# Kernel tuning notes

Hardware: AMD Instinct MI355X
Metric: run time of the kernel (lower is better)

The kernel has to match this reference:

```python
import jax, jax.numpy as jnp
import numpy as np

B, S, R = 8, 4096, 512
E, K, ATOMS, XAR, TOPK = 64, 256, 16, 3, 2
TEMP = 1.0


def setup_inputs() -> dict:
    key = jax.random.key(0)
    k0, k1, k2, k3, k4 = jax.random.split(key, 5)
    x_latent = jax.random.normal(k0, (B, S, R), jnp.float32)
    router_w = jax.random.normal(k1, (E, R), jnp.float32) * (1.0 / np.sqrt(R))
    atoms = jax.random.normal(k2, (E, ATOMS, R), jnp.float32) * 0.01
    combo_weights = jax.random.uniform(k3, (E, K, XAR), jnp.float32) * 0.5 + 0.25
    combo_logits = jax.random.normal(k4, (E, K, XAR, ATOMS), jnp.float32) * 0.01
    return {"x_latent": x_latent, "router_w": router_w, "atoms": atoms,
            "combo_weights": combo_weights, "combo_logits": combo_logits}


def _expert_centroids(atoms, combo_weights, combo_logits):
    # Hard codeword path (vectorized over experts):
    # sign atoms -> pick argmax atom per (k, xor slot) -> weight -> sum -> sign -> mean over k
    binary = jnp.sign(atoms)                                   # [E, A, R]
    # softmax(logits/t) then argmax == argmax(logits) (monotone)
    idx = jnp.argmax(combo_logits, axis=-1)                    # [E, K, XAR]
    sel = binary[jnp.arange(E)[:, None, None], idx]            # [E, K, XAR, R]
    codewords = jnp.sign((sel * combo_weights[..., None]).sum(axis=2))  # [E, K, R]
    return codewords.mean(axis=1)                              # [E, R]


def reference(x_latent, router_w, atoms, combo_weights, combo_logits):
    t = max(TEMP, 0.1)
    router_logits = jnp.einsum('bsr,er->bse', x_latent, router_w)   # [B, S, E]
    probs_t = jax.nn.softmax(router_logits / t, axis=-1)
    gates, expert_ids = jax.lax.top_k(probs_t, TOPK)                # [B, S, 2]
    gates = gates / gates.sum(axis=-1, keepdims=True)

    centroids = _expert_centroids(atoms, combo_weights, combo_logits)  # [E, R]

    # aux load-balancing loss (uses untempered softmax)
    router_prob = jax.nn.softmax(router_logits, axis=-1)
    aux_loss = E * jnp.sum(router_prob.mean(axis=(0, 1)) *
                           (router_prob > 0).astype(x_latent.dtype).mean(axis=(0, 1)))

    # dense per-expert gate = sum over topk slots of gate * (id == e), then combine with centroids
    dense_gates = (jax.nn.one_hot(expert_ids, E, dtype=gates.dtype) *
                   gates[..., None]).sum(axis=-2)                    # [B, S, E]
    combined = jnp.einsum('bse,er->bsr', dense_gates, centroids)     # [B, S, R]
    return combined, aux_loss
```

## Files before the change

### kernel.cpp

```cpp
#include <hip/hip_runtime.h>
#include <math.h>

#define TOKENS 32768
#define RDIM 512
#define NEXP 64
#define NK 256
#define LDQ 136
#define PSTR 67
#define TAU 4.0e-3f

typedef unsigned short u16;
typedef float f32x4 __attribute__((ext_vector_type(4)));
typedef short s16x8 __attribute__((ext_vector_type(8)));

#define MFMA_B16(a, b, c) __builtin_amdgcn_mfma_f32_16x16x32_bf16(a, b, c, 0, 0, 0)

__device__ __forceinline__ void split_pack(float4 v, unsigned& h01, unsigned& h23,
                                           unsigned& l01, unsigned& l23) {
    unsigned u0 = __float_as_uint(v.x), u1 = __float_as_uint(v.y);
    unsigned u2 = __float_as_uint(v.z), u3 = __float_as_uint(v.w);
    float r0 = v.x - __uint_as_float(u0 & 0xFFFF0000u);
    float r1 = v.y - __uint_as_float(u1 & 0xFFFF0000u);
    float r2 = v.z - __uint_as_float(u2 & 0xFFFF0000u);
    float r3 = v.w - __uint_as_float(u3 & 0xFFFF0000u);
    h01 = (u0 >> 16) | (u1 & 0xFFFF0000u);
    h23 = (u2 >> 16) | (u3 & 0xFFFF0000u);
    l01 = (__float_as_uint(r0) >> 16) | (__float_as_uint(r1) & 0xFFFF0000u);
    l23 = (__float_as_uint(r2) >> 16) | (__float_as_uint(r3) & 0xFFFF0000u);
}

__device__ __forceinline__ void split8(float4 a, float4 b, s16x8& hi, s16x8& lo) {
    union U { unsigned u[4]; s16x8 v; };
    U H, L;
    split_pack(a, H.u[0], H.u[1], L.u[0], L.u[1]);
    split_pack(b, H.u[2], H.u[3], L.u[2], L.u[3]);
    hi = H.v; lo = L.v;
}

__device__ __forceinline__ void centroid_body(
    int e, int half, int tid,
    const float* __restrict__ atoms, const float* __restrict__ cw,
    const float* __restrict__ cl, float* __restrict__ cent, unsigned* pack)
{
    {
        const int k = tid;
        unsigned u = 0;
        float w3[3];
        #pragma unroll
        for (int xx = 0; xx < 3; ++xx) {
            const float* cp = cl + ((((size_t)e * NK + k) * 3 + xx) << 4);
            float v[16];
            *(float4*)(v + 0)  = *(const float4*)(cp + 0);
            *(float4*)(v + 4)  = *(const float4*)(cp + 4);
            *(float4*)(v + 8)  = *(const float4*)(cp + 8);
            *(float4*)(v + 12) = *(const float4*)(cp + 12);
            float best = v[0]; int bi = 0;
            #pragma unroll
            for (int a = 1; a < 16; ++a) {
                if (v[a] > best) { best = v[a]; bi = a; }
            }
            u |= (unsigned)bi << (4 * xx);
            w3[xx] = cw[((size_t)e * NK + k) * 3 + xx];
        }
        unsigned lut = 0;
        #pragma unroll
        for (int c = 0; c < 8; ++c) {
            float val = ((c & 1) ? -w3[0] : w3[0])
                      + ((c & 2) ? -w3[1] : w3[1])
                      + ((c & 4) ? -w3[2] : w3[2]);
            lut |= (val < 0.f ? 1u : 0u) << c;
        }
        pack[k] = u | (lut << 16);
    }

    const int r = half * 256 + tid;
    unsigned B0 = 0;
    #pragma unroll
    for (int a = 0; a < 16; ++a)
        B0 |= (atoms[((size_t)e * 16 + a) * RDIM + r] < 0.f ? 1u : 0u) << a;
    __syncthreads();

    int n0 = 0;
    #pragma unroll 2
    for (int k = 0; k < NK; k += 8) {
        unsigned pk8[8];
        #pragma unroll
        for (int j = 0; j < 8; ++j) pk8[j] = pack[k + j];
        #pragma unroll
        for (int j = 0; j < 8; ++j) {
            unsigned u  = pk8[j];
            unsigned i0 = u & 15u, i1 = (u >> 4) & 15u, i2 = (u >> 8) & 15u;
            unsigned c0 = ((B0 >> i0) & 1u) | (((B0 >> i1) & 1u) << 1) | (((B0 >> i2) & 1u) << 2);
            n0 += (u >> (16 + c0)) & 1u;
        }
    }
    cent[(size_t)e * RDIM + r] = 1.f - (float)n0 * (1.f / 128.f);
}

__global__ __launch_bounds__(256) void centroid_pack_kernel(
    const float* __restrict__ atoms,
    const float* __restrict__ cw,
    const float* __restrict__ cl,
    const float* __restrict__ w,
    float* __restrict__ cent,
    u16* __restrict__ pk_hi,
    u16* __restrict__ pk_lo,
    float* __restrict__ aux_sum,
    unsigned* __restrict__ aux_cnt)
{
    __shared__ unsigned pack[NK];
    const int tid = threadIdx.x;
    if (blockIdx.x == 0 && tid < 64) { aux_sum[tid] = 0.f; aux_cnt[tid] = 0u; }

    if (blockIdx.x < 128) {
        centroid_body(blockIdx.x >> 1, blockIdx.x & 1, tid, atoms, cw, cl, cent, pack);
    } else {
        const int gid = (blockIdx.x - 128) * 256 + tid;
        const int row = gid >> 7;
        const int k0  = (gid & 127) * 4;
        const int g   = k0 >> 5, kg = (k0 >> 3) & 3, j = k0 & 7;
        const int idx = ((g * 4 + kg) * 64 + row) * 8 + j;
        float4 wv = *(const float4*)(w + (size_t)row * RDIM + k0);
        unsigned h01, h23, l01, l23;
        split_pack(wv, h01, h23, l01, l23);
        *(uint2*)&pk_hi[idx] = make_uint2(h01, h23);
        *(uint2*)&pk_lo[idx] = make_uint2(l01, l23);
    }
}

__global__ __launch_bounds__(128, 4) void moe_fast(
    const float* __restrict__ x,
    const u16* __restrict__ pk_hi,
    const u16* __restrict__ pk_lo,
    const float* __restrict__ w,
    const float* __restrict__ cent,
    float* __restrict__ out,
    float* __restrict__ aux_sum,
    unsigned* __restrict__ aux_cnt)
{
    __shared__ float P[32 * PSTR];
    __shared__ float candv[32 * 13];
    __shared__ int   candi[32 * 13];
    __shared__ float qsum[32 * 5];
    __shared__ float gateL[32 * 4];
    __shared__ float s_aux[64];
    __shared__ unsigned s_cnt[64];

    const int tid  = threadIdx.x;
    const int lane = tid & 63;
    const int wv   = tid >> 6;
    const int l15  = lane & 15;
    const int kq   = lane >> 4;
    const int kgrp = kq << 3;
    const int tok0 = blockIdx.x * 32;

    if (tid < 64) { s_aux[tid] = 0.f; s_cnt[tid] = 0u; }

    f32x4 acc[4];
    #pragma unroll
    for (int nt = 0; nt < 4; ++nt) acc[nt] = (f32x4){0.f, 0.f, 0.f, 0.f};

    const float* xlane = x + (size_t)(tok0 + wv * 16 + l15) * RDIM + kgrp;
    const int fbase = kq * 512 + l15 * 8;

    float4 pA[2], pB[2];
    pA[0] = *(const float4*)(xlane);      pB[0] = *(const float4*)(xlane + 4);
    pA[1] = *(const float4*)(xlane + 32); pB[1] = *(const float4*)(xlane + 36);

    #pragma unroll
    for (int g = 0; g < 16; ++g) {
        s16x8 ah, al;
        split8(pA[g & 1], pB[g & 1], ah, al);
        if (g + 2 < 16) {
            const float* nx = xlane + (g + 2) * 32;
            pA[g & 1] = *(const float4*)(nx);
            pB[g & 1] = *(const float4*)(nx + 4);
        }
        const u16* ph = pk_hi + g * 2048 + fbase;
        const u16* pl = pk_lo + g * 2048 + fbase;
        #pragma unroll
        for (int nt = 0; nt < 4; ++nt) {
            s16x8 bh = *(const s16x8*)(ph + nt * 128);
            s16x8 bl = *(const s16x8*)(pl + nt * 128);
            acc[nt] = MFMA_B16(ah, bh, acc[nt]);
            acc[nt] = MFMA_B16(ah, bl, acc[nt]);
            acc[nt] = MFMA_B16(al, bh, acc[nt]);
        }
    }

    #pragma unroll
    for (int nt = 0; nt < 4; ++nt)
        #pragma unroll
        for (int i = 0; i < 4; ++i)
            P[(wv * 16 + (kq << 2) + i) * PSTR + nt * 16 + l15] = acc[nt][i];
    __syncthreads();

    const int tt = tid & 31;
    const int ss = tid >> 5;
    float v[16];
    #pragma unroll
    for (int j = 0; j < 16; ++j) v[j] = P[tt * PSTR + ss * 16 + j];

    float m1 = -INFINITY, m2 = -INFINITY, m3 = -INFINITY;
    int   i1 = NEXP, i2 = NEXP, i3 = NEXP;
    #pragma unroll
    for (int j = 0; j < 16; ++j) {
        float val = v[j]; int e = ss * 16 + j;
        if (val > m1)      { m3 = m2; i3 = i2; m2 = m1; i2 = i1; m1 = val; i1 = e; }
        else if (val > m2) { m3 = m2; i3 = i2; m2 = val; i2 = e; }
        else if (val > m3) { m3 = val; i3 = e; }
    }
    candv[tt * 13 + ss * 3 + 0] = m1; candi[tt * 13 + ss * 3 + 0] = i1;
    candv[tt * 13 + ss * 3 + 1] = m2; candi[tt * 13 + ss * 3 + 1] = i2;
    candv[tt * 13 + ss * 3 + 2] = m3; candi[tt * 13 + ss * 3 + 2] = i3;
    __syncthreads();

    m1 = m2 = m3 = -INFINITY; i1 = i2 = i3 = NEXP;
    #pragma unroll
    for (int q = 0; q < 12; ++q) {
        float val = candv[tt * 13 + q]; int e = candi[tt * 13 + q];
        if (val > m1)      { m3 = m2; i3 = i2; m2 = m1; i2 = i1; m1 = val; i1 = e; }
        else if (val > m2) { m3 = m2; i3 = i2; m2 = val; i2 = e; }
        else if (val > m3) { m3 = val; i3 = e; }
    }

    float ex[16]; float ps = 0.f;
    #pragma unroll
    for (int j = 0; j < 16; ++j) { ex[j] = __expf(v[j] - m1); ps += ex[j]; }
    qsum[tt * 5 + ss] = ps;

    if (wv == 0) {
        if (lane < 32) {
            const float ed  = __expf(m2 - m1);
            const float inv = 1.f / (1.f + ed);
            gateL[tt * 4 + 0] = inv;
            gateL[tt * 4 + 1] = ed * inv;
            ((int*)gateL)[tt * 4 + 2] = i1;
            ((int*)gateL)[tt * 4 + 3] = i2;
        }
        unsigned long long bmask = __ballot(lane < 32 && (m2 - m3 < TAU));
        while (bmask) {
            const int f = __ffsll(bmask) - 1;
            bmask &= bmask - 1;
            int id3[3];
            id3[0] = __shfl(i1, f); id3[1] = __shfl(i2, f); id3[2] = __shfl(i3, f);
            const float* xrow = x + (size_t)(tok0 + f) * RDIM + lane * 8;
            float4 a0 = *(const float4*)(xrow);
            float4 a1 = *(const float4*)(xrow + 4);
            float d[3];
            #pragma unroll
            for (int jj = 0; jj < 3; ++jj) {
                const float* wrow = w + (size_t)id3[jj] * RDIM + lane * 8;
                float4 b0 = *(const float4*)(wrow);
                float4 b1 = *(const float4*)(wrow + 4);
                float p = a0.x * b0.x;
                p = fmaf(a0.y, b0.y, p); p = fmaf(a0.z, b0.z, p); p = fmaf(a0.w, b0.w, p);
                p = fmaf(a1.x, b1.x, p); p = fmaf(a1.y, b1.y, p);
                p = fmaf(a1.z, b1.z, p); p = fmaf(a1.w, b1.w, p);
                #pragma unroll
                for (int off = 32; off; off >>= 1) p += __shfl_xor(p, off);
                d[jj] = p;
            }
            int b = 0;
            if (d[1] > d[0] || (d[1] == d[0] && id3[1] < id3[0])) b = 1;
            if (d[2] > d[b] || (d[2] == d[b] && id3[2] < id3[b])) b = 2;
            int sec;
            if (b == 0)      sec = (d[1] > d[2] || (d[1] == d[2] && id3[1] < id3[2])) ? 1 : 2;
            else if (b == 1) sec = (d[0] > d[2] || (d[0] == d[2] && id3[0] < id3[2])) ? 0 : 2;
            else             sec = (d[0] > d[1] || (d[0] == d[1] && id3[0] < id3[1])) ? 0 : 1;
            if (lane == f) {
                const float ed  = __expf(d[sec] - d[b]);
                const float inv = 1.f / (1.f + ed);
                gateL[f * 4 + 0] = inv;
                gateL[f * 4 + 1] = ed * inv;
                ((int*)gateL)[f * 4 + 2] = id3[b];
                ((int*)gateL)[f * 4 + 3] = id3[sec];
            }
        }
    }
    __syncthreads();

    float Z = 0.f;
    #pragma unroll
    for (int k = 0; k < 4; ++k) Z += qsum[tt * 5 + k];
    const float invZ = 1.f / Z;
    #pragma unroll
    for (int j = 0; j < 16; ++j) P[tt * PSTR + ss * 16 + j] = ex[j] * invZ;
    __syncthreads();

    {
        const int e = tid & 63, tq = tid >> 6;
        float s = 0.f; unsigned cn = 0u;
        #pragma unroll
        for (int t = 0; t < 16; ++t) {
            float pv = P[(tq * 16 + t) * PSTR + e];
            s += pv; cn += (pv > 0.f) ? 1u : 0u;
        }
        atomicAdd(&s_aux[e], s);
        atomicAdd(&s_cnt[e], cn);
    }
    __syncthreads();
    if (tid < 64) {
        atomicAdd(aux_sum + tid, s_aux[tid]);
        atomicAdd(aux_cnt + tid, s_cnt[tid]);
    }

    {
        const int e = lane;
        #pragma unroll
        for (int s2 = 0; s2 < 16; ++s2) {
            const int t2 = wv * 16 + s2;
            float4 g4 = *(float4*)&gateL[t2 * 4];
            const float g1 = g4.x, g2 = g4.y;
            const int e1 = __float_as_int(g4.z), e2 = __float_as_int(g4.w);
            const float4* c1 = (const float4*)(cent + (size_t)e1 * RDIM);
            const float4* c2 = (const float4*)(cent + (size_t)e2 * RDIM);
            float4* op = (float4*)(out + (size_t)(tok0 + t2) * RDIM);
            float4 A0 = c1[e],      Bb0 = c2[e];
            float4 A1 = c1[e + 64], Bb1 = c2[e + 64];
            float4 o0, o1;
            o0.x = fmaf(g1, A0.x, g2 * Bb0.x); o0.y = fmaf(g1, A0.y, g2 * Bb0.y);
            o0.z = fmaf(g1, A0.z, g2 * Bb0.z); o0.w = fmaf(g1, A0.w, g2 * Bb0.w);
            o1.x = fmaf(g1, A1.x, g2 * Bb1.x); o1.y = fmaf(g1, A1.y, g2 * Bb1.y);
            o1.z = fmaf(g1, A1.z, g2 * Bb1.z); o1.w = fmaf(g1, A1.w, g2 * Bb1.w);
            op[e]      = o0;
            op[e + 64] = o1;
        }
    }
}

__global__ __launch_bounds__(256) void centroid_kernel(
    const float* __restrict__ atoms,
    const float* __restrict__ cw,
    const float* __restrict__ cl,
    float* __restrict__ cent,
    float* __restrict__ aux_sum,
    unsigned* __restrict__ aux_cnt)
{
    __shared__ unsigned pack[NK];
    const int tid = threadIdx.x;
    if (blockIdx.x == 0 && tid < 64) { aux_sum[tid] = 0.f; aux_cnt[tid] = 0u; }
    centroid_body(blockIdx.x >> 1, blockIdx.x & 1, tid, atoms, cw, cl, cent, pack);
}

__global__ __launch_bounds__(256, 4) void moe_main(
    const float* __restrict__ x,
    const float* __restrict__ w,
    const float* __restrict__ cent,
    float* __restrict__ out,
    float* __restrict__ aux_sum,
    unsigned* __restrict__ aux_cnt)
{
    __shared__ u16 wlds[2 * 64 * LDQ];
    u16* whi = wlds;
    u16* wlo = wlds + 64 * LDQ;
    float* P     = (float*)wlds;
    float* candv = P + 64 * PSTR;
    int*   candi = (int*)(candv + 64 * 13);
    float* qsum  = (float*)(candi + 64 * 13);
    float* gateL = qsum + 64 * 5;
    __shared__ float s_aux[64];
    __shared__ unsigned s_cnt[64];

    const int tid  = threadIdx.x;
    const int lane = tid & 63;
    const int wave = tid >> 6;
    const int l15  = lane & 15;
    const int kgrp = (lane >> 4) << 3;
    const int tok0 = blockIdx.x * 64;

    if (tid < 64) { s_aux[tid] = 0.f; s_cnt[tid] = 0u; }

    f32x4 acc[4];
    #pragma unroll
    for (int nt = 0; nt < 4; ++nt) acc[nt] = (f32x4){0.f, 0.f, 0.f, 0.f};

    const float* xlane = x + (size_t)(tok0 + wave * 16 + l15) * RDIM + kgrp;
    const int wrow = tid >> 2;
    const int wseg = tid & 3;
    const float* wg = w + (size_t)wrow * RDIM + wseg * 32;
    const int woff = wrow * LDQ + wseg * 32;

    float4 preA[4], preB[4];
    #pragma unroll
    for (int i = 0; i < 4; ++i) {
        preA[i] = *(const float4*)(xlane + i * 32);
        preB[i] = *(const float4*)(xlane + i * 32 + 4);
    }

    #pragma unroll
    for (int q = 0; q < 4; ++q) {
        if (q) __syncthreads();
        {
            const float* wq = wg + q * 128;
            uint2 h2[2], l2[2];
            #pragma unroll
            for (int j = 0; j < 8; ++j) {
                float4 wvv = *(const float4*)(wq + j * 4);
                split_pack(wvv, h2[j & 1].x, h2[j & 1].y, l2[j & 1].x, l2[j & 1].y);
                if (j & 1) {
                    *(uint4*)&whi[woff + (j - 1) * 4] =
                        make_uint4(h2[0].x, h2[0].y, h2[1].x, h2[1].y);
                    *(uint4*)&wlo[woff + (j - 1) * 4] =
                        make_uint4(l2[0].x, l2[0].y, l2[1].x, l2[1].y);
                }
            }
        }
        __syncthreads();

        #pragma unroll
        for (int kb = 0; kb < 4; ++kb) {
            const int g = q * 4 + kb;
            s16x8 ah, al;
            split8(preA[g & 3], preB[g & 3], ah, al);
            if (g + 4 < 16) {
                const float* nx = xlane + (g + 4) * 32;
                preA[g & 3] = *(const float4*)(nx);
                preB[g & 3] = *(const float4*)(nx + 4);
            }
            const int kl = kb * 32 + kgrp;
            #pragma unroll
            for (int nt = 0; nt < 4; ++nt) {
                const int brow = nt * 16 + l15;
                s16x8 bh = *(const s16x8*)&whi[brow * LDQ + kl];
                s16x8 bl = *(const s16x8*)&wlo[brow * LDQ + kl];
                acc[nt] = MFMA_B16(ah, bh, acc[nt]);
                acc[nt] = MFMA_B16(ah, bl, acc[nt]);
                acc[nt] = MFMA_B16(al, bh, acc[nt]);
            }
        }
    }

    __syncthreads();
    #pragma unroll
    for (int nt = 0; nt < 4; ++nt)
        #pragma unroll
        for (int i = 0; i < 4; ++i)
            P[(wave * 16 + ((lane >> 4) << 2) + i) * PSTR + nt * 16 + l15] = acc[nt][i];
    __syncthreads();

    const int tt = tid & 63;
    const int ss = tid >> 6;
    float v[16];
    #pragma unroll
    for (int j = 0; j < 16; ++j) v[j] = P[tt * PSTR + ss * 16 + j];

    float m1 = -INFINITY, m2 = -INFINITY, m3 = -INFINITY;
    int   i1 = NEXP, i2 = NEXP, i3 = NEXP;
    #pragma unroll
    for (int j = 0; j < 16; ++j) {
        float val = v[j]; int e = ss * 16 + j;
        if (val > m1)      { m3 = m2; i3 = i2; m2 = m1; i2 = i1; m1 = val; i1 = e; }
        else if (val > m2) { m3 = m2; i3 = i2; m2 = val; i2 = e; }
        else if (val > m3) { m3 = val; i3 = e; }
    }
    candv[tt * 13 + ss * 3 + 0] = m1; candi[tt * 13 + ss * 3 + 0] = i1;
    candv[tt * 13 + ss * 3 + 1] = m2; candi[tt * 13 + ss * 3 + 1] = i2;
    candv[tt * 13 + ss * 3 + 2] = m3; candi[tt * 13 + ss * 3 + 2] = i3;
    __syncthreads();

    m1 = m2 = m3 = -INFINITY; i1 = i2 = i3 = NEXP;
    #pragma unroll
    for (int q = 0; q < 12; ++q) {
        float val = candv[tt * 13 + q]; int e = candi[tt * 13 + q];
        if (val > m1)      { m3 = m2; i3 = i2; m2 = m1; i2 = i1; m1 = val; i1 = e; }
        else if (val > m2) { m3 = m2; i3 = i2; m2 = val; i2 = e; }
        else if (val > m3) { m3 = val; i3 = e; }
    }

    float ex[16]; float ps = 0.f;
    #pragma unroll
    for (int j = 0; j < 16; ++j) { ex[j] = __expf(v[j] - m1); ps += ex[j]; }
    qsum[tt * 5 + ss] = ps;

    if (ss == 0) {
        {
            const float ed  = __expf(m2 - m1);
            const float inv = 1.f / (1.f + ed);
            gateL[tt * 4 + 0] = inv;
            gateL[tt * 4 + 1] = ed * inv;
            ((int*)gateL)[tt * 4 + 2] = i1;
            ((int*)gateL)[tt * 4 + 3] = i2;
        }
        unsigned long long bmask = __ballot(m2 - m3 < TAU);
        while (bmask) {
            const int f = __ffsll(bmask) - 1;
            bmask &= bmask - 1;
            int id3[3];
            id3[0] = __shfl(i1, f); id3[1] = __shfl(i2, f); id3[2] = __shfl(i3, f);
            const float* xrow = x + (size_t)(tok0 + f) * RDIM + lane * 8;
            float4 a0 = *(const float4*)(xrow);
            float4 a1 = *(const float4*)(xrow + 4);
            float d[3];
            #pragma unroll
            for (int jj = 0; jj < 3; ++jj) {
                const float* wrow2 = w + (size_t)id3[jj] * RDIM + lane * 8;
                float4 b0 = *(const float4*)(wrow2);
                float4 b1 = *(const float4*)(wrow2 + 4);
                float p = a0.x * b0.x;
                p = fmaf(a0.y, b0.y, p); p = fmaf(a0.z, b0.z, p); p = fmaf(a0.w, b0.w, p);
                p = fmaf(a1.x, b1.x, p); p = fmaf(a1.y, b1.y, p);
                p = fmaf(a1.z, b1.z, p); p = fmaf(a1.w, b1.w, p);
                #pragma unroll
                for (int off = 32; off; off >>= 1) p += __shfl_xor(p, off);
                d[jj] = p;
            }
            int b = 0;
            if (d[1] > d[0] || (d[1] == d[0] && id3[1] < id3[0])) b = 1;
            if (d[2] > d[b] || (d[2] == d[b] && id3[2] < id3[b])) b = 2;
            int sec;
            if (b == 0)      sec = (d[1] > d[2] || (d[1] == d[2] && id3[1] < id3[2])) ? 1 : 2;
            else if (b == 1) sec = (d[0] > d[2] || (d[0] == d[2] && id3[0] < id3[2])) ? 0 : 2;
            else             sec = (d[0] > d[1] || (d[0] == d[1] && id3[0] < id3[1])) ? 0 : 1;
            if (lane == f) {
                const float ed  = __expf(d[sec] - d[b]);
                const float inv = 1.f / (1.f + ed);
                gateL[f * 4 + 0] = inv;
                gateL[f * 4 + 1] = ed * inv;
                ((int*)gateL)[f * 4 + 2] = id3[b];
                ((int*)gateL)[f * 4 + 3] = id3[sec];
            }
        }
    }
    __syncthreads();

    float Z = 0.f;
    #pragma unroll
    for (int k = 0; k < 4; ++k) Z += qsum[tt * 5 + k];
    const float invZ = 1.f / Z;
    #pragma unroll
    for (int j = 0; j < 16; ++j) P[tt * PSTR + ss * 16 + j] = ex[j] * invZ;
    __syncthreads();

    {
        const int e = tid & 63, tq = tid >> 6;
        float s = 0.f; unsigned cn = 0u;
        #pragma unroll
        for (int t = 0; t < 16; ++t) {
            float pv = P[(tq * 16 + t) * PSTR + e];
            s += pv; cn += (pv > 0.f) ? 1u : 0u;
        }
        atomicAdd(&s_aux[e], s);
        atomicAdd(&s_cnt[e], cn);
    }
    __syncthreads();
    if (tid < 64) {
        atomicAdd(aux_sum + tid, s_aux[tid]);
        atomicAdd(aux_cnt + tid, s_cnt[tid]);
    }

    {
        const int e = lane;
        #pragma unroll
        for (int s2 = 0; s2 < 16; ++s2) {
            const int t2 = wave * 16 + s2;
            float4 g4 = *(float4*)&gateL[t2 * 4];
            const float g1 = g4.x, g2 = g4.y;
            const int e1 = __float_as_int(g4.z), e2 = __float_as_int(g4.w);
            const float4* c1 = (const float4*)(cent + (size_t)e1 * RDIM);
            const float4* c2 = (const float4*)(cent + (size_t)e2 * RDIM);
            float4* op = (float4*)(out + (size_t)(tok0 + t2) * RDIM);
            float4 A0 = c1[e],      Bb0 = c2[e];
            float4 A1 = c1[e + 64], Bb1 = c2[e + 64];
            float4 o0, o1;
            o0.x = fmaf(g1, A0.x, g2 * Bb0.x); o0.y = fmaf(g1, A0.y, g2 * Bb0.y);
            o0.z = fmaf(g1, A0.z, g2 * Bb0.z); o0.w = fmaf(g1, A0.w, g2 * Bb0.w);
            o1.x = fmaf(g1, A1.x, g2 * Bb1.x); o1.y = fmaf(g1, A1.y, g2 * Bb1.y);
            o1.z = fmaf(g1, A1.z, g2 * Bb1.z); o1.w = fmaf(g1, A1.w, g2 * Bb1.w);
            op[e]      = o0;
            op[e + 64] = o1;
        }
    }
}

__global__ __launch_bounds__(64) void aux_kernel(
    const float* __restrict__ sums,
    const unsigned* __restrict__ cnts,
    float* __restrict__ out_aux)
{
    const int e = threadIdx.x;
    float v = (sums[e] * (1.f / (float)TOKENS)) * ((float)cnts[e] * (1.f / (float)TOKENS));
    #pragma unroll
    for (int off = 32; off; off >>= 1) v += __shfl_xor(v, off);
    if (e == 0) out_aux[0] = (float)NEXP * v;
}

extern "C" void kernel_launch(void* const* d_in, const int* in_sizes, int n_in,
                              void* d_out, int out_size, void* d_ws, size_t ws_size,
                              hipStream_t stream) {
    const float* x     = (const float*)d_in[0];
    const float* rw    = (const float*)d_in[1];
    const float* atoms = (const float*)d_in[2];
    const float* cwts  = (const float*)d_in[3];
    const float* clog  = (const float*)d_in[4];
    float* out = (float*)d_out;
    float* out_aux = out + (size_t)TOKENS * RDIM;

    float*    aux_sum = (float*)d_ws;
    unsigned* aux_cnt = (unsigned*)((char*)d_ws + 256);
    float*    cent    = (float*)((char*)d_ws + 512);
    u16*      pk_hi   = (u16*)((char*)d_ws + 512 + 131072);
    u16*      pk_lo   = (u16*)((char*)d_ws + 512 + 131072 + 65536);
    const bool fast = ws_size >= (size_t)(512 + 131072 + 2 * 65536);

    if (fast) {
        centroid_pack_kernel<<<160, 256, 0, stream>>>(atoms, cwts, clog, rw, cent,
                                                      pk_hi, pk_lo, aux_sum, aux_cnt);
        moe_fast<<<1024, 128, 0, stream>>>(x, pk_hi, pk_lo, rw, cent, out, aux_sum, aux_cnt);
    } else {
        centroid_kernel<<<128, 256, 0, stream>>>(atoms, cwts, clog, cent, aux_sum, aux_cnt);
        moe_main<<<512, 256, 0, stream>>>(x, rw, cent, out, aux_sum, aux_cnt);
    }
    aux_kernel<<<1, 64, 0, stream>>>(aux_sum, aux_cnt, out_aux);
}
```

Before: 168.1 us.

## Split router GEMM expert columns across waves with 16-token blocks

Blocks now cover 16 tokens instead of 32, and each of four waves computes a 16-expert slice of the router logits rather than all 64 experts for its own tokens. The grid grows to 2048 blocks of 256 threads to raise occupancy and shorten each wave's serial MFMA chain. Top-k, softmax and the near-tie refinement now run in a single wave per block, and exponentials are recomputed instead of kept in registers. The cost is that all four waves load the same x rows, relying on cache to absorb the duplicate reads, and the other three waves sit idle during the top-k phase.

```diff
diff --git a/kernel.cpp b/kernel.cpp
--- a/kernel.cpp
+++ b/kernel.cpp
@@ -128,7 +128,7 @@
     }
 }
 
-__global__ __launch_bounds__(128, 4) void moe_fast(
+__global__ __launch_bounds__(256, 8) void moe_fast2(
     const float* __restrict__ x,
     const u16* __restrict__ pk_hi,
     const u16* __restrict__ pk_lo,
@@ -138,11 +138,11 @@
     float* __restrict__ aux_sum,
     unsigned* __restrict__ aux_cnt)
 {
-    __shared__ float P[32 * PSTR];
-    __shared__ float candv[32 * 13];
-    __shared__ int   candi[32 * 13];
-    __shared__ float qsum[32 * 5];
-    __shared__ float gateL[32 * 4];
+    __shared__ float P[16 * PSTR];
+    __shared__ float candv[16 * 13];
+    __shared__ int   candi[16 * 13];
+    __shared__ float qsum[16 * 4];
+    __shared__ float gateL[16 * 4];
     __shared__ float s_aux[64];
     __shared__ unsigned s_cnt[64];
 
@@ -152,16 +152,14 @@
     const int l15  = lane & 15;
     const int kq   = lane >> 4;
     const int kgrp = kq << 3;
-    const int tok0 = blockIdx.x * 32;
+    const int tok0 = blockIdx.x * 16;
 
     if (tid < 64) { s_aux[tid] = 0.f; s_cnt[tid] = 0u; }
 
-    f32x4 acc[4];
-    #pragma unroll
-    for (int nt = 0; nt < 4; ++nt) acc[nt] = (f32x4){0.f, 0.f, 0.f, 0.f};
-
-    const float* xlane = x + (size_t)(tok0 + wv * 16 + l15) * RDIM + kgrp;
-    const int fbase = kq * 512 + l15 * 8;
+    f32x4 acc = (f32x4){0.f, 0.f, 0.f, 0.f};
+
+    const float* xlane = x + (size_t)(tok0 + l15) * RDIM + kgrp;
+    const int fbase = kq * 512 + (wv * 16 + l15) * 8;
 
     float4 pA[2], pB[2];
     pA[0] = *(const float4*)(xlane);      pB[0] = *(const float4*)(xlane + 4);
@@ -178,59 +176,53 @@
         }
         const u16* ph = pk_hi + g * 2048 + fbase;
         const u16* pl = pk_lo + g * 2048 + fbase;
-        #pragma unroll
-        for (int nt = 0; nt < 4; ++nt) {
-            s16x8 bh = *(const s16x8*)(ph + nt * 128);
-            s16x8 bl = *(const s16x8*)(pl + nt * 128);
-            acc[nt] = MFMA_B16(ah, bh, acc[nt]);
-            acc[nt] = MFMA_B16(ah, bl, acc[nt]);
-            acc[nt] = MFMA_B16(al, bh, acc[nt]);
-        }
-    }
-
-    #pragma unroll
-    for (int nt = 0; nt < 4; ++nt)
-        #pragma unroll
-        for (int i = 0; i < 4; ++i)
-            P[(wv * 16 + (kq << 2) + i) * PSTR + nt * 16 + l15] = acc[nt][i];
-    __syncthreads();
-
-    const int tt = tid & 31;
-    const int ss = tid >> 5;
-    float v[16];
-    #pragma unroll
-    for (int j = 0; j < 16; ++j) v[j] = P[tt * PSTR + ss * 16 + j];
-
-    float m1 = -INFINITY, m2 = -INFINITY, m3 = -INFINITY;
-    int   i1 = NEXP, i2 = NEXP, i3 = NEXP;
-    #pragma unroll
-    for (int j = 0; j < 16; ++j) {
-        float val = v[j]; int e = ss * 16 + j;
-        if (val > m1)      { m3 = m2; i3 = i2; m2 = m1; i2 = i1; m1 = val; i1 = e; }
-        else if (val > m2) { m3 = m2; i3 = i2; m2 = val; i2 = e; }
-        else if (val > m3) { m3 = val; i3 = e; }
-    }
-    candv[tt * 13 + ss * 3 + 0] = m1; candi[tt * 13 + ss * 3 + 0] = i1;
-    candv[tt * 13 + ss * 3 + 1] = m2; candi[tt * 13 + ss * 3 + 1] = i2;
-    candv[tt * 13 + ss * 3 + 2] = m3; candi[tt * 13 + ss * 3 + 2] = i3;
-    __syncthreads();
-
-    m1 = m2 = m3 = -INFINITY; i1 = i2 = i3 = NEXP;
-    #pragma unroll
-    for (int q = 0; q < 12; ++q) {
-        float val = candv[tt * 13 + q]; int e = candi[tt * 13 + q];
-        if (val > m1)      { m3 = m2; i3 = i2; m2 = m1; i2 = i1; m1 = val; i1 = e; }
-        else if (val > m2) { m3 = m2; i3 = i2; m2 = val; i2 = e; }
-        else if (val > m3) { m3 = val; i3 = e; }
-    }
-
-    float ex[16]; float ps = 0.f;
-    #pragma unroll
-    for (int j = 0; j < 16; ++j) { ex[j] = __expf(v[j] - m1); ps += ex[j]; }
-    qsum[tt * 5 + ss] = ps;
-
-    if (wv == 0) {
-        if (lane < 32) {
+        s16x8 bh = *(const s16x8*)ph;
+        s16x8 bl = *(const s16x8*)pl;
+        acc = MFMA_B16(ah, bh, acc);
+        acc = MFMA_B16(ah, bl, acc);
+        acc = MFMA_B16(al, bh, acc);
+    }
+
+    #pragma unroll
+    for (int i = 0; i < 4; ++i)
+        P[(kq * 4 + i) * PSTR + wv * 16 + l15] = acc[i];
+    __syncthreads();
+
+    if (tid < 64) {
+        const int tt = lane & 15;
+        const int ss = lane >> 4;
+        float v[16];
+        #pragma unroll
+        for (int j = 0; j < 16; ++j) v[j] = P[tt * PSTR + ss * 16 + j];
+
+        float m1 = -INFINITY, m2 = -INFINITY, m3 = -INFINITY;
+        int   i1 = NEXP, i2 = NEXP, i3 = NEXP;
+        #pragma unroll
+        for (int j = 0; j < 16; ++j) {
+            float val = v[j]; int e = ss * 16 + j;
+            if (val > m1)      { m3 = m2; i3 = i2; m2 = m1; i2 = i1; m1 = val; i1 = e; }
+            else if (val > m2) { m3 = m2; i3 = i2; m2 = val; i2 = e; }
+            else if (val > m3) { m3 = val; i3 = e; }
+        }
+        candv[tt * 13 + ss * 3 + 0] = m1; candi[tt * 13 + ss * 3 + 0] = i1;
+        candv[tt * 13 + ss * 3 + 1] = m2; candi[tt * 13 + ss * 3 + 1] = i2;
+        candv[tt * 13 + ss * 3 + 2] = m3; candi[tt * 13 + ss * 3 + 2] = i3;
+
+        m1 = m2 = m3 = -INFINITY; i1 = i2 = i3 = NEXP;
+        #pragma unroll
+        for (int q = 0; q < 12; ++q) {
+            float val = candv[tt * 13 + q]; int e = candi[tt * 13 + q];
+            if (val > m1)      { m3 = m2; i3 = i2; m2 = m1; i2 = i1; m1 = val; i1 = e; }
+            else if (val > m2) { m3 = m2; i3 = i2; m2 = val; i2 = e; }
+            else if (val > m3) { m3 = val; i3 = e; }
+        }
+
+        float ps = 0.f;
+        #pragma unroll
+        for (int j = 0; j < 16; ++j) ps += __expf(v[j] - m1);
+        qsum[tt * 4 + ss] = ps;
+
+        if (ss == 0) {
             const float ed  = __expf(m2 - m1);
             const float inv = 1.f / (1.f + ed);
             gateL[tt * 4 + 0] = inv;
@@ -238,7 +230,7 @@
             ((int*)gateL)[tt * 4 + 2] = i1;
             ((int*)gateL)[tt * 4 + 3] = i2;
         }
-        unsigned long long bmask = __ballot(lane < 32 && (m2 - m3 < TAU));
+        unsigned long long bmask = __ballot(ss == 0 && (m2 - m3 < TAU));
         while (bmask) {
             const int f = __ffsll(bmask) - 1;
             bmask &= bmask - 1;
@@ -277,23 +269,21 @@
                 ((int*)gateL)[f * 4 + 3] = id3[sec];
             }
         }
-    }
-    __syncthreads();
-
-    float Z = 0.f;
-    #pragma unroll
-    for (int k = 0; k < 4; ++k) Z += qsum[tt * 5 + k];
-    const float invZ = 1.f / Z;
-    #pragma unroll
-    for (int j = 0; j < 16; ++j) P[tt * PSTR + ss * 16 + j] = ex[j] * invZ;
+
+        float Z = qsum[tt * 4 + 0] + qsum[tt * 4 + 1] + qsum[tt * 4 + 2] + qsum[tt * 4 + 3];
+        const float invZ = 1.f / Z;
+        #pragma unroll
+        for (int j = 0; j < 16; ++j)
+            P[tt * PSTR + ss * 16 + j] = __expf(v[j] - m1) * invZ;
+    }
     __syncthreads();
 
     {
         const int e = tid & 63, tq = tid >> 6;
         float s = 0.f; unsigned cn = 0u;
         #pragma unroll
-        for (int t = 0; t < 16; ++t) {
-            float pv = P[(tq * 16 + t) * PSTR + e];
+        for (int t = 0; t < 4; ++t) {
+            float pv = P[(tq * 4 + t) * PSTR + e];
             s += pv; cn += (pv > 0.f) ? 1u : 0u;
         }
         atomicAdd(&s_aux[e], s);
@@ -308,8 +298,8 @@
     {
         const int e = lane;
         #pragma unroll
-        for (int s2 = 0; s2 < 16; ++s2) {
-            const int t2 = wv * 16 + s2;
+        for (int s2 = 0; s2 < 4; ++s2) {
+            const int t2 = wv * 4 + s2;
             float4 g4 = *(float4*)&gateL[t2 * 4];
             const float g1 = g4.x, g2 = g4.y;
             const int e1 = __float_as_int(g4.z), e2 = __float_as_int(g4.w);
@@ -606,7 +596,7 @@
     if (fast) {
         centroid_pack_kernel<<<160, 256, 0, stream>>>(atoms, cwts, clog, rw, cent,
                                                       pk_hi, pk_lo, aux_sum, aux_cnt);
-        moe_fast<<<1024, 128, 0, stream>>>(x, pk_hi, pk_lo, rw, cent, out, aux_sum, aux_cnt);
+        moe_fast2<<<2048, 256, 0, stream>>>(x, pk_hi, pk_lo, rw, cent, out, aux_sum, aux_cnt);
     } else {
         centroid_kernel<<<128, 256, 0, stream>>>(atoms, cwts, clog, cent, aux_sum, aux_cnt);
         moe_main<<<512, 256, 0, stream>>>(x, rw, cent, out, aux_sum, aux_cnt);
```

Result: slower. 207.2 us (+23.3%).

## Split router GEMM experts across two waves and deepen operand prefetch

Applied to the files above, without the earlier changes.

Each 32-token block now runs with 256 threads instead of 128. Pairs of waves share a 16-token group, and each wave of the pair computes 32 of the 64 expert logits, so every wave issues half the MFMAs. The x rows are prefetched four stages ahead, and the packed bf16 router-weight fragments are double-buffered in registers, so more memory latency is hidden. The softmax, top-k, aux and output epilogues are re-indexed to spread over the larger block. The cost is that x is now loaded twice per token group, and each block uses more registers and shared memory, which may lower occupancy.

```diff
diff --git a/kernel.cpp b/kernel.cpp
--- a/kernel.cpp
+++ b/kernel.cpp
@@ -128,7 +128,7 @@
     }
 }
 
-__global__ __launch_bounds__(128, 4) void moe_fast(
+__global__ __launch_bounds__(256, 4) void moe_fast3(
     const float* __restrict__ x,
     const u16* __restrict__ pk_hi,
     const u16* __restrict__ pk_lo,
@@ -139,9 +139,9 @@
     unsigned* __restrict__ aux_cnt)
 {
     __shared__ float P[32 * PSTR];
-    __shared__ float candv[32 * 13];
-    __shared__ int   candi[32 * 13];
-    __shared__ float qsum[32 * 5];
+    __shared__ float candv[32 * 25];
+    __shared__ int   candi[32 * 25];
+    __shared__ float qsum[32 * 9];
     __shared__ float gateL[32 * 4];
     __shared__ float s_aux[64];
     __shared__ unsigned s_cnt[64];
@@ -149,6 +149,8 @@
     const int tid  = threadIdx.x;
     const int lane = tid & 63;
     const int wv   = tid >> 6;
+    const int tokG = wv >> 1;
+    const int expG = wv & 1;
     const int l15  = lane & 15;
     const int kq   = lane >> 4;
     const int kgrp = kq << 3;
@@ -156,78 +158,95 @@
 
     if (tid < 64) { s_aux[tid] = 0.f; s_cnt[tid] = 0u; }
 
-    f32x4 acc[4];
-    #pragma unroll
-    for (int nt = 0; nt < 4; ++nt) acc[nt] = (f32x4){0.f, 0.f, 0.f, 0.f};
-
-    const float* xlane = x + (size_t)(tok0 + wv * 16 + l15) * RDIM + kgrp;
-    const int fbase = kq * 512 + l15 * 8;
-
-    float4 pA[2], pB[2];
-    pA[0] = *(const float4*)(xlane);      pB[0] = *(const float4*)(xlane + 4);
-    pA[1] = *(const float4*)(xlane + 32); pB[1] = *(const float4*)(xlane + 36);
+    f32x4 acc[2];
+    acc[0] = (f32x4){0.f, 0.f, 0.f, 0.f};
+    acc[1] = (f32x4){0.f, 0.f, 0.f, 0.f};
+
+    const float* xlane = x + (size_t)(tok0 + tokG * 16 + l15) * RDIM + kgrp;
+    const int fb0 = kq * 512 + (expG * 32 + l15) * 8;
+    const int fb1 = fb0 + 128;
+
+    float4 preA[4], preB[4];
+    #pragma unroll
+    for (int i = 0; i < 4; ++i) {
+        preA[i] = *(const float4*)(xlane + i * 32);
+        preB[i] = *(const float4*)(xlane + i * 32 + 4);
+    }
+    s16x8 pbh[2][2], pbl[2][2];
+    #pragma unroll
+    for (int p = 0; p < 2; ++p) {
+        pbh[p][0] = *(const s16x8*)(pk_hi + p * 2048 + fb0);
+        pbh[p][1] = *(const s16x8*)(pk_hi + p * 2048 + fb1);
+        pbl[p][0] = *(const s16x8*)(pk_lo + p * 2048 + fb0);
+        pbl[p][1] = *(const s16x8*)(pk_lo + p * 2048 + fb1);
+    }
 
     #pragma unroll
     for (int g = 0; g < 16; ++g) {
         s16x8 ah, al;
-        split8(pA[g & 1], pB[g & 1], ah, al);
+        split8(preA[g & 3], preB[g & 3], ah, al);
+        if (g + 4 < 16) {
+            const float* nx = xlane + (g + 4) * 32;
+            preA[g & 3] = *(const float4*)(nx);
+            preB[g & 3] = *(const float4*)(nx + 4);
+        }
+        s16x8 bh0 = pbh[g & 1][0], bl0 = pbl[g & 1][0];
+        s16x8 bh1 = pbh[g & 1][1], bl1 = pbl[g & 1][1];
         if (g + 2 < 16) {
-            const float* nx = xlane + (g + 2) * 32;
-            pA[g & 1] = *(const float4*)(nx);
-            pB[g & 1] = *(const float4*)(nx + 4);
-        }
-        const u16* ph = pk_hi + g * 2048 + fbase;
-        const u16* pl = pk_lo + g * 2048 + fbase;
-        #pragma unroll
-        for (int nt = 0; nt < 4; ++nt) {
-            s16x8 bh = *(const s16x8*)(ph + nt * 128);
-            s16x8 bl = *(const s16x8*)(pl + nt * 128);
-            acc[nt] = MFMA_B16(ah, bh, acc[nt]);
-            acc[nt] = MFMA_B16(ah, bl, acc[nt]);
-            acc[nt] = MFMA_B16(al, bh, acc[nt]);
-        }
-    }
-
-    #pragma unroll
-    for (int nt = 0; nt < 4; ++nt)
+            const int o = (g + 2) * 2048;
+            pbh[g & 1][0] = *(const s16x8*)(pk_hi + o + fb0);
+            pbh[g & 1][1] = *(const s16x8*)(pk_hi + o + fb1);
+            pbl[g & 1][0] = *(const s16x8*)(pk_lo + o + fb0);
+            pbl[g & 1][1] = *(const s16x8*)(pk_lo + o + fb1);
+        }
+        acc[0] = MFMA_B16(ah, bh0, acc[0]);
+        acc[0] = MFMA_B16(ah, bl0, acc[0]);
+        acc[0] = MFMA_B16(al, bh0, acc[0]);
+        acc[1] = MFMA_B16(ah, bh1, acc[1]);
+        acc[1] = MFMA_B16(ah, bl1, acc[1]);
+        acc[1] = MFMA_B16(al, bh1, acc[1]);
+    }
+
+    #pragma unroll
+    for (int nt = 0; nt < 2; ++nt)
         #pragma unroll
         for (int i = 0; i < 4; ++i)
-            P[(wv * 16 + (kq << 2) + i) * PSTR + nt * 16 + l15] = acc[nt][i];
+            P[(tokG * 16 + kq * 4 + i) * PSTR + expG * 32 + nt * 16 + l15] = acc[nt][i];
     __syncthreads();
 
     const int tt = tid & 31;
     const int ss = tid >> 5;
-    float v[16];
-    #pragma unroll
-    for (int j = 0; j < 16; ++j) v[j] = P[tt * PSTR + ss * 16 + j];
+    float v[8];
+    #pragma unroll
+    for (int j = 0; j < 8; ++j) v[j] = P[tt * PSTR + ss * 8 + j];
 
     float m1 = -INFINITY, m2 = -INFINITY, m3 = -INFINITY;
     int   i1 = NEXP, i2 = NEXP, i3 = NEXP;
     #pragma unroll
-    for (int j = 0; j < 16; ++j) {
-        float val = v[j]; int e = ss * 16 + j;
+    for (int j = 0; j < 8; ++j) {
+        float val = v[j]; int e = ss * 8 + j;
         if (val > m1)      { m3 = m2; i3 = i2; m2 = m1; i2 = i1; m1 = val; i1 = e; }
         else if (val > m2) { m3 = m2; i3 = i2; m2 = val; i2 = e; }
         else if (val > m3) { m3 = val; i3 = e; }
     }
-    candv[tt * 13 + ss * 3 + 0] = m1; candi[tt * 13 + ss * 3 + 0] = i1;
-    candv[tt * 13 + ss * 3 + 1] = m2; candi[tt * 13 + ss * 3 + 1] = i2;
-    candv[tt * 13 + ss * 3 + 2] = m3; candi[tt * 13 + ss * 3 + 2] = i3;
+    candv[tt * 25 + ss * 3 + 0] = m1; candi[tt * 25 + ss * 3 + 0] = i1;
+    candv[tt * 25 + ss * 3 + 1] = m2; candi[tt * 25 + ss * 3 + 1] = i2;
+    candv[tt * 25 + ss * 3 + 2] = m3; candi[tt * 25 + ss * 3 + 2] = i3;
     __syncthreads();
 
     m1 = m2 = m3 = -INFINITY; i1 = i2 = i3 = NEXP;
     #pragma unroll
-    for (int q = 0; q < 12; ++q) {
-        float val = candv[tt * 13 + q]; int e = candi[tt * 13 + q];
+    for (int q = 0; q < 24; ++q) {
+        float val = candv[tt * 25 + q]; int e = candi[tt * 25 + q];
         if (val > m1)      { m3 = m2; i3 = i2; m2 = m1; i2 = i1; m1 = val; i1 = e; }
         else if (val > m2) { m3 = m2; i3 = i2; m2 = val; i2 = e; }
         else if (val > m3) { m3 = val; i3 = e; }
     }
 
-    float ex[16]; float ps = 0.f;
-    #pragma unroll
-    for (int j = 0; j < 16; ++j) { ex[j] = __expf(v[j] - m1); ps += ex[j]; }
-    qsum[tt * 5 + ss] = ps;
+    float ex[8]; float ps = 0.f;
+    #pragma unroll
+    for (int j = 0; j < 8; ++j) { ex[j] = __expf(v[j] - m1); ps += ex[j]; }
+    qsum[tt * 9 + ss] = ps;
 
     if (wv == 0) {
         if (lane < 32) {
@@ -282,18 +301,18 @@
 
     float Z = 0.f;
     #pragma unroll
-    for (int k = 0; k < 4; ++k) Z += qsum[tt * 5 + k];
+    for (int k = 0; k < 8; ++k) Z += qsum[tt * 9 + k];
     const float invZ = 1.f / Z;
     #pragma unroll
-    for (int j = 0; j < 16; ++j) P[tt * PSTR + ss * 16 + j] = ex[j] * invZ;
+    for (int j = 0; j < 8; ++j) P[tt * PSTR + ss * 8 + j] = ex[j] * invZ;
     __syncthreads();
 
     {
         const int e = tid & 63, tq = tid >> 6;
         float s = 0.f; unsigned cn = 0u;
         #pragma unroll
-        for (int t = 0; t < 16; ++t) {
-            float pv = P[(tq * 16 + t) * PSTR + e];
+        for (int t = 0; t < 8; ++t) {
+            float pv = P[(tq * 8 + t) * PSTR + e];
             s += pv; cn += (pv > 0.f) ? 1u : 0u;
         }
         atomicAdd(&s_aux[e], s);
@@ -308,8 +327,8 @@
     {
         const int e = lane;
         #pragma unroll
-        for (int s2 = 0; s2 < 16; ++s2) {
-            const int t2 = wv * 16 + s2;
+        for (int s2 = 0; s2 < 8; ++s2) {
+            const int t2 = wv * 8 + s2;
             float4 g4 = *(float4*)&gateL[t2 * 4];
             const float g1 = g4.x, g2 = g4.y;
             const int e1 = __float_as_int(g4.z), e2 = __float_as_int(g4.w);
@@ -606,7 +625,7 @@
     if (fast) {
         centroid_pack_kernel<<<160, 256, 0, stream>>>(atoms, cwts, clog, rw, cent,
                                                       pk_hi, pk_lo, aux_sum, aux_cnt);
-        moe_fast<<<1024, 128, 0, stream>>>(x, pk_hi, pk_lo, rw, cent, out, aux_sum, aux_cnt);
+        moe_fast3<<<1024, 256, 0, stream>>>(x, pk_hi, pk_lo, rw, cent, out, aux_sum, aux_cnt);
     } else {
         centroid_kernel<<<128, 256, 0, stream>>>(atoms, cwts, clog, cent, aux_sum, aux_cnt);
         moe_main<<<512, 256, 0, stream>>>(x, rw, cent, out, aux_sum, aux_cnt);
```

New measurement: 170.4 us. Within noise of the previous version (+1.4%).
